# Kernel optimization log

Measured on AMD Instinct MI355X. Metric: run time of the kernel, lower is better.

Reference implementation:

```python
import jax, jax.numpy as jnp
import numpy as np

B, N, M, C, K = 4, 4096, 4096, 64, 32
RADIUS = 0.1
EPS = 1e-5


def setup_inputs() -> dict:
    key = jax.random.key(0)
    ks = jax.random.split(key, 32)
    inp = {
        "query_xyz": jax.random.uniform(ks[0], (B, N, 3), jnp.float32),
        "support_xyz": jax.random.uniform(ks[1], (B, M, 3), jnp.float32),
        "query_mask": jax.random.randint(ks[2], (B, N), 0, 2, jnp.int32),
        "support_mask": jax.random.randint(ks[3], (B, M), 0, 2, jnp.int32),
        "support_features": jax.random.normal(ks[4], (B, C, M), jnp.float32),
    }
    names = ["theta1", "theta2", "phi", "psi", "alpha", "gamma1", "gamma2"]
    in_ch = {"theta1": 3}
    for j, nm in enumerate(names):
        inp[f"W_{nm}"] = jax.random.normal(ks[5 + j], (C, in_ch.get(nm, C)), jnp.float32) * 0.05
        inp[f"b_{nm}"] = jax.random.normal(ks[12 + j], (C,), jnp.float32) * 0.05
    for j, nm in enumerate(["theta", "gamma"]):
        inp[f"g_{nm}"] = 1.0 + 0.1 * jax.random.normal(ks[19 + 2 * j], (C,), jnp.float32)
        inp[f"be_{nm}"] = 0.1 * jax.random.normal(ks[20 + 2 * j], (C,), jnp.float32)
        inp[f"rm_{nm}"] = jnp.zeros((C,), jnp.float32)
        inp[f"rv_{nm}"] = jnp.ones((C,), jnp.float32)
    return inp


def _conv(W, b, x):
    # 1x1 Conv2d: channelwise linear on [B, C_in, N, K]
    return jnp.einsum('oc,bcnk->bonk', W, x) + b[None, :, None, None]


def _bn(x, g, be, rm, rv):
    # BatchNorm2d, inference form with running stats
    inv = g / jnp.sqrt(rv + EPS)
    return x * inv[None, :, None, None] + (be - rm * inv)[None, :, None, None]


def _forward(query_xyz, support_xyz, query_mask, support_mask, support_features, P):
    Bq, Nq = query_xyz.shape[:2]
    # pairwise squared distances [B, N, M]; masked support pushed to +inf
    d2 = jnp.sum((query_xyz[:, :, None, :] - support_xyz[:, None, :, :]) ** 2, axis=-1)
    d2 = jnp.where(support_mask[:, None, :] > 0, d2, jnp.inf)
    # ball query as K-nearest-within-radius
    neg, idx = jax.lax.top_k(-d2, K)                    # idx: [B, N, K]
    nbr_mask = (-neg) <= RADIUS ** 2                    # valid-neighbor mask
    flat = idx.reshape(Bq, Nq * K)
    x_j = jnp.take_along_axis(support_features, flat[:, None, :], axis=2).reshape(Bq, -1, Nq, K)
    g_xyz = jnp.take_along_axis(support_xyz, flat[:, :, None], axis=1).reshape(Bq, Nq, K, 3)
    # normalize_xyz=True -> offsets divided by radius; layout [B, 3, N, K]
    pos = ((g_xyz - query_xyz[:, :, None, :]) / RADIUS).transpose(0, 3, 1, 2)
    # nearest-neighbor query for x_i [B, C, N]
    idx_nn = jnp.argmin(d2, axis=-1)
    x_i = jnp.take_along_axis(support_features, idx_nn[:, None, :], axis=2)
    # positional encoding delta
    delta = jax.nn.relu(_bn(_conv(P['W_theta2'], P['b_theta2'],
                                  _conv(P['W_theta1'], P['b_theta1'], pos)),
                            P['g_theta'], P['be_theta'], P['rm_theta'], P['rv_theta']))
    lin_i = _conv(P['W_phi'], P['b_phi'], x_i[..., None])   # [B,C,N,1], broadcast over K
    lin_j = _conv(P['W_psi'], P['b_psi'], x_j)
    rel = lin_i - lin_j + delta
    rel = jax.nn.relu(_bn(_conv(P['W_gamma2'], P['b_gamma2'],
                                _conv(P['W_gamma1'], P['b_gamma1'], rel)),
                          P['g_gamma'], P['be_gamma'], P['rm_gamma'], P['rv_gamma']))
    weights = jax.nn.softmax(rel, axis=-1)                   # softmax over neighbor axis
    feats = _conv(P['W_alpha'], P['b_alpha'], x_j) + delta
    fmask = nbr_mask.astype(feats.dtype) + (1.0 - query_mask.astype(feats.dtype))[:, :, None]
    feats = feats * fmask[:, None, :, :]
    return jnp.sum(weights * feats, axis=-1)                 # [B, C, N]


def reference(query_xyz, support_xyz, query_mask, support_mask, support_features,
              W_theta1, b_theta1, W_theta2, b_theta2, W_phi, b_phi, W_psi, b_psi,
              W_alpha, b_alpha, W_gamma1, b_gamma1, W_gamma2, b_gamma2,
              g_theta, be_theta, rm_theta, rv_theta, g_gamma, be_gamma, rm_gamma, rv_gamma):
    P = dict(locals())
    return _forward(query_xyz, support_xyz, query_mask, support_mask, support_features, P)
```

## Files before the change

### kernel.cpp

```cpp
#include <hip/hip_runtime.h>
#include <cstdint>
#include <cstddef>

#define NN 4096
#define MM 4096
#define CC 64
#define KK 32
#define INF_F __builtin_huge_valf()

#define SC 2304
#define CCAP 2560

typedef __bf16 bf16x8 __attribute__((ext_vector_type(8)));
typedef __bf16 bf16x4 __attribute__((ext_vector_type(4)));
typedef float f32x16 __attribute__((ext_vector_type(16)));

#define NFRAG 40
#define NPRE 24
#define ASTRIDE 68
#define ESTRIDE 36

#define WFENCE() asm volatile("s_waitcnt lgkmcnt(0)" ::: "memory")


__device__ __forceinline__ f32x16 zero16() {
  f32x16 z;
#pragma unroll
  for (int i = 0; i < 16; ++i) z[i] = 0.0f;
  return z;
}

__device__ __forceinline__ void conv1(const bf16x8* Wr, int conv,
                                      const bf16x8* B4, f32x16& a0, f32x16& a1) {
#pragma unroll
  for (int s = 0; s < 4; ++s) {
    a0 = __builtin_amdgcn_mfma_f32_32x32x16_bf16(Wr[(conv * 2 + 0) * 4 + s], B4[s], a0, 0, 0, 0);
    a1 = __builtin_amdgcn_mfma_f32_32x32x16_bf16(Wr[(conv * 2 + 1) * 4 + s], B4[s], a1, 0, 0, 0);
  }
}

__device__ __forceinline__ void conv1g(const bf16x8* __restrict__ Wf, int conv, int lane,
                                       const bf16x8* B4, f32x16& a0, f32x16& a1) {
#pragma unroll
  for (int s = 0; s < 4; ++s) {
    const bf16x8 w0 = Wf[((conv * 2 + 0) * 4 + s) * 64 + lane];
    const bf16x8 w1 = Wf[((conv * 2 + 1) * 4 + s) * 64 + lane];
    a0 = __builtin_amdgcn_mfma_f32_32x32x16_bf16(w0, B4[s], a0, 0, 0, 0);
    a1 = __builtin_amdgcn_mfma_f32_32x32x16_bf16(w1, B4[s], a1, 0, 0, 0);
  }
}

__device__ __forceinline__ void sort64(float& v, int& i, int lane) {
#pragma unroll
  for (int k = 2; k <= 64; k <<= 1) {
#pragma unroll
    for (int j = k >> 1; j > 0; j >>= 1) {
      const float ov = __shfl_xor(v, j);
      const int oi = __shfl_xor(i, j);
      const bool up = ((lane & k) == 0);
      const bool lower = ((lane & j) == 0);
      const bool take = (up == lower) ? (ov < v) : (ov > v);
      if (take) { v = ov; i = oi; }
    }
  }
}

__device__ __forceinline__ void insert_cands(float vv, int ii, float& sv, int& si,
                                             float& cmax, int lane) {
  unsigned long long cand = __ballot(vv < cmax);
  while (cand) {
    const int src = __ffsll((unsigned long long)cand) - 1;
    cand &= cand - 1;
    const float dc = __shfl(vv, src);
    if (dc < cmax) {
      const int im = __shfl(ii, src);
      const float up_s = __shfl_up(sv, 1);
      const int up_i = __shfl_up(si, 1);
      const bool pg = sv > dc;
      const bool pgu = (lane > 0) && (up_s > dc);
      const float ns = pg ? (pgu ? up_s : dc) : sv;
      const int ni = pg ? (pgu ? up_i : im) : si;
      if (lane < 32) { sv = ns; si = ni; }
      cmax = __shfl(sv, 31);
    }
  }
}

__global__ void pt_setup(const float* __restrict__ sf, const float* __restrict__ sxyz,
                         const int* __restrict__ smask,
                         const float* __restrict__ Wpsi, const float* __restrict__ W2,
                         const float* __restrict__ Wg1, const float* __restrict__ Wg2,
                         const float* __restrict__ Wa, const float* __restrict__ Wphi,
                         const float* __restrict__ gT, const float* __restrict__ beT,
                         const float* __restrict__ rmT, const float* __restrict__ rvT,
                         const float* __restrict__ gG, const float* __restrict__ beG,
                         const float* __restrict__ rmG, const float* __restrict__ rvG,
                         const float* __restrict__ b2, const float* __restrict__ bg1,
                         const float* __restrict__ bg2, const float* __restrict__ ba,
                         __bf16* __restrict__ ftb, float4* __restrict__ sx4,
                         float4* __restrict__ cpts, __bf16* __restrict__ Wpack,
                         float* __restrict__ WphiT, float4* __restrict__ eo,
                         float4* __restrict__ bo) {
  const int blk = blockIdx.x;
  const int tid = threadIdx.x;

  if (blk < 64) {
    const int b = blk >> 4;
    const int m = ((blk & 15) << 8) + tid;
    float v[CC];
#pragma unroll
    for (int c = 0; c < CC; ++c) v[c] = sf[((size_t)(b * CC + c)) * MM + m];
    bf16x8* db = (bf16x8*)(ftb + ((size_t)(b * MM + m)) * CC);
#pragma unroll
    for (int i = 0; i < CC / 8; ++i) {
      bf16x8 t;
#pragma unroll
      for (int j = 0; j < 8; ++j) t[j] = (__bf16)v[8 * i + j];
      db[i] = t;
    }
    const size_t g = (size_t)(b * MM + m);
    sx4[g] = make_float4(sxyz[g * 3 + 0], sxyz[g * 3 + 1], sxyz[g * 3 + 2], 0.0f);
    return;
  }

  if (blk < 68) {
    __shared__ int lcount;
    const int b = blk - 64;
    const int lane = tid & 63;
    if (tid == 0) lcount = 0;
    __syncthreads();
    float4* dst = cpts + (size_t)b * CCAP;
#pragma unroll 1
    for (int r = 0; r < 16; ++r) {
      const int m = r * 256 + tid;
      const size_t g = (size_t)b * MM + m;
      const bool valid = smask[g] > 0;
      float x = 0, y = 0, z = 0;
      if (valid) { x = sxyz[g * 3 + 0]; y = sxyz[g * 3 + 1]; z = sxyz[g * 3 + 2]; }
      const unsigned long long mask = __ballot(valid);
      const int pre = (int)__popcll(mask & ((1ull << lane) - 1ull));
      int wbase = 0;
      if (lane == 0) wbase = atomicAdd(&lcount, (int)__popcll(mask));
      wbase = __shfl(wbase, 0);
      if (valid) dst[wbase + pre] = make_float4(x, y, z, __int_as_float(m));
    }
    __syncthreads();
    const int cnt = lcount;
    for (int i = cnt + tid; i < SC; i += 256)
      dst[i] = make_float4(1e4f, 1e4f, 1e4f, __int_as_float(0));
    return;
  }

  const int t = (blk - 68) * 256 + tid;
  if (t < NFRAG * 64) {
    const int lane = t & 63;
    const int fi = t >> 6;
    const int s = fi & 3;
    const int mt = (fi >> 2) & 1;
    const int conv = fi >> 3;
    const float* W = conv == 0 ? Wpsi : conv == 1 ? W2 : conv == 2 ? Wg1 : conv == 3 ? Wg2 : Wa;
    const int m = mt * 32 + (lane & 31);
    const int k0 = s * 16 + (lane >> 5) * 8;
    bf16x8 vh;
#pragma unroll
    for (int j = 0; j < 8; ++j) vh[j] = (__bf16)W[m * CC + k0 + j];
    ((bf16x8*)Wpack)[fi * 64 + lane] = vh;
    return;
  }
  const int t2 = t - NFRAG * 64;
  if (t2 < CC * CC) {
    WphiT[t2] = Wphi[(t2 & 63) * CC + (t2 >> 6)];
    return;
  }
  const int o = t2 - CC * CC;
  if (o < CC) {
    const float invT = gT[o] / sqrtf(rvT[o] + 1e-5f);
    const float invG = gG[o] / sqrtf(rvG[o] + 1e-5f);
    eo[o] = make_float4(invT, beT[o] - rmT[o] * invT, invG, beG[o] - rmG[o] * invG);
    bo[o] = make_float4(b2[o], bg1[o], bg2[o], ba[o]);
  }
}

__global__ void pt_knn(const float* __restrict__ qxyz, const float4* __restrict__ cpts,
                       const __bf16* __restrict__ ftb,
                       const float* __restrict__ WphiT, const float* __restrict__ bphi,
                       const float* __restrict__ bpsi,
                       int* __restrict__ oidx, unsigned* __restrict__ ovalid,
                       float* __restrict__ lin) {
  const int lane = threadIdx.x & 63;
  const int qi = blockIdx.x * 4 + (threadIdx.x >> 6);
  const int b = qi >> 12;
  const float qx = qxyz[qi * 3 + 0];
  const float qy = qxyz[qi * 3 + 1];
  const float qz = qxyz[qi * 3 + 2];
  const float4* sb = cpts + (size_t)b * CCAP;

  float v0 = INF_F, v1 = INF_F, v2 = INF_F, v3 = INF_F;
  int i0 = 0, i1 = 0, i2 = 0, i3 = 0;
#pragma unroll 1
  for (int j = 0; j < 36; j += 4) {
    float4 P[4];
#pragma unroll
    for (int u = 0; u < 4; ++u) P[u] = sb[(j + u) * 64 + lane];
#pragma unroll
    for (int u = 0; u < 4; ++u) {
      const float dx = P[u].x - qx, dy = P[u].y - qy, dz = P[u].z - qz;
      const float d = dx * dx + dy * dy + dz * dz;
      const int m = __float_as_int(P[u].w);
      const bool c3 = d < v3, c2 = d < v2, c1 = d < v1, c0 = d < v0;
      v3 = c3 ? (c2 ? v2 : d) : v3;  i3 = c3 ? (c2 ? i2 : m) : i3;
      v2 = c2 ? (c1 ? v1 : d) : v2;  i2 = c2 ? (c1 ? i1 : m) : i2;
      v1 = c1 ? (c0 ? v0 : d) : v1;  i1 = c1 ? (c0 ? i0 : m) : i1;
      v0 = c0 ? d : v0;              i0 = c0 ? m : i0;
    }
  }

  float sv = v0;
  int si = i0;
  sort64(sv, si, lane);
  float cmax = __shfl(sv, 31);
  insert_cands(v1, i1, sv, si, cmax, lane);
  insert_cands(v2, i2, sv, si, cmax, lane);
  insert_cands(v3, i3, sv, si, cmax, lane);

  if (__ballot(v3 < cmax)) {
    {
      const float4 p = sb[lane];
      const float dx = p.x - qx, dy = p.y - qy, dz = p.z - qz;
      float v = dx * dx + dy * dy + dz * dz;
      int id = __float_as_int(p.w);
      sort64(v, id, lane);
      sv = v; si = id;
    }
    cmax = __shfl(sv, 31);
    for (int m0 = 64; m0 < SC; m0 += 64) {
      const float4 p = sb[m0 + lane];
      const float dx = p.x - qx, dy = p.y - qy, dz = p.z - qz;
      const float d = dx * dx + dy * dy + dz * dz;
      insert_cands(d, __float_as_int(p.w), sv, si, cmax, lane);
    }
  }

  if (lane < 32) oidx[(size_t)qi * KK + lane] = si;
  const unsigned long long vb = __ballot((lane < 32) && (sv <= 0.01f));
  if (lane == 0) ovalid[qi] = (unsigned)(vb & 0xffffffffull);

  const int nnb = __shfl(si, 0);
  const bf16x8* xr = (const bf16x8*)(ftb + ((size_t)(b * MM + nnb)) * CC);
  float a = bphi[lane] - bpsi[lane];
#pragma unroll
  for (int i = 0; i < 8; ++i) {
    const bf16x8 xv = xr[i];
#pragma unroll
    for (int j = 0; j < 8; ++j) a += WphiT[(8 * i + j) * CC + lane] * (float)xv[j];
  }
  lin[qi * CC + lane] = a;
}

__launch_bounds__(256, 3)
__global__ void pt_fused(
    const float* __restrict__ qxyz, const float4* __restrict__ sx4,
    const int* __restrict__ qmask, const __bf16* __restrict__ ftb,
    const int* __restrict__ kidx, const unsigned* __restrict__ kvalid,
    const float* __restrict__ lin,
    const float* __restrict__ W1, const float* __restrict__ b1,
    const __bf16* __restrict__ Wpack, const float4* __restrict__ eo,
    const float4* __restrict__ bo, float* __restrict__ out) {
  __shared__ float EPI[4][CC * ESTRIDE];
  __shared__ float4 sEO[CC], sBO[CC];
  const int wid = threadIdx.x >> 6;
  const int lane = threadIdx.x & 63;
  const int g = lane >> 5;
  const int col = lane & 31;
  const int q = blockIdx.x * 4 + wid;
  const int b = q >> 12;
  const int nq = q & (NN - 1);
  float* epi = EPI[wid];
  __bf16* act = (__bf16*)epi;
  const bf16x8* Wf = (const bf16x8*)Wpack;

  bf16x8 Wr[NPRE];
#pragma unroll
  for (int f = 0; f < NPRE; ++f) Wr[f] = Wf[f * 64 + lane];

  sEO[lane] = eo[lane];
  sBO[lane] = bo[lane];

  const int idx = kidx[q * KK + col];
  const float fm = (float)((kvalid[q] >> col) & 1u) + 1.0f - (float)qmask[q];

  bf16x8 Xb[4];
  {
    const __bf16* ftq = ftb + ((size_t)(b * MM + idx)) * CC;
#pragma unroll
    for (int s = 0; s < 4; ++s) Xb[s] = *(const bf16x8*)(ftq + s * 16 + g * 8);
  }

  bf16x8 Tb[4];
  {
    const float qx = qxyz[q * 3 + 0], qy = qxyz[q * 3 + 1], qz = qxyz[q * 3 + 2];
    const float4 pj = sx4[(size_t)b * MM + idx];
    const float p0 = (pj.x - qx) * 10.0f;
    const float p1 = (pj.y - qy) * 10.0f;
    const float p2 = (pj.z - qz) * 10.0f;
#pragma unroll
    for (int s = 0; s < 4; ++s) {
      bf16x8 t;
#pragma unroll
      for (int j = 0; j < 8; ++j) {
        const int c = s * 16 + g * 8 + j;
        t[j] = (__bf16)(b1[c] + W1[c * 3 + 0] * p0 + W1[c * 3 + 1] * p1 + W1[c * 3 + 2] * p2);
      }
      Tb[s] = t;
    }
  }
  WFENCE();

  float DELv[32];
  {
    f32x16 aT0 = zero16(), aT1 = zero16();
    conv1(Wr, 1, Tb, aT0, aT1);
#pragma unroll
    for (int mt = 0; mt < 2; ++mt)
#pragma unroll
      for (int t = 0; t < 4; ++t)
#pragma unroll
        for (int i = 0; i < 4; ++i) {
          const int r = t * 4 + i;
          const int o = mt * 32 + 8 * t + 4 * g + i;
          const float4 e = sEO[o];
          DELv[mt * 16 + r] = fmaxf(((mt ? aT1[r] : aT0[r]) + sBO[o].x) * e.x + e.y, 0.0f);
        }
  }

  {
    f32x16 aP0 = zero16(), aP1 = zero16();
    conv1(Wr, 0, Xb, aP0, aP1);
#pragma unroll
    for (int mt = 0; mt < 2; ++mt)
#pragma unroll
      for (int t = 0; t < 4; ++t) {
        const int ob = mt * 32 + 8 * t + 4 * g;
        const float4 lv = *(const float4*)(lin + q * CC + ob);
        const float lva[4] = {lv.x, lv.y, lv.z, lv.w};
        bf16x4 w;
#pragma unroll
        for (int i = 0; i < 4; ++i) {
          const int r = t * 4 + i;
          w[i] = (__bf16)(lva[i] - (mt ? aP1[r] : aP0[r]) + DELv[mt * 16 + r]);
        }
        *(bf16x4*)(act + col * ASTRIDE + ob) = w;
      }
  }
  WFENCE();

  {
    bf16x8 Rb[4];
#pragma unroll
    for (int s = 0; s < 4; ++s) {
      const bf16x4 lo = *(const bf16x4*)(act + col * ASTRIDE + s * 16 + g * 8);
      const bf16x4 hi = *(const bf16x4*)(act + col * ASTRIDE + s * 16 + g * 8 + 4);
      Rb[s] = bf16x8{lo[0], lo[1], lo[2], lo[3], hi[0], hi[1], hi[2], hi[3]};
    }
    f32x16 a0 = zero16(), a1 = zero16();
    conv1(Wr, 2, Rb, a0, a1);
#pragma unroll
    for (int mt = 0; mt < 2; ++mt)
#pragma unroll
      for (int t = 0; t < 4; ++t) {
        const int ob = mt * 32 + 8 * t + 4 * g;
        bf16x4 w;
#pragma unroll
        for (int i = 0; i < 4; ++i) {
          const int r = t * 4 + i;
          w[i] = (__bf16)((mt ? a1[r] : a0[r]) + sBO[ob + i].y);
        }
        *(bf16x4*)(act + col * ASTRIDE + ob) = w;
      }
  }
  WFENCE();

  f32x16 h0 = zero16(), h1 = zero16();
  {
    bf16x8 Rb[4];
#pragma unroll
    for (int s = 0; s < 4; ++s) {
      const bf16x4 lo = *(const bf16x4*)(act + col * ASTRIDE + s * 16 + g * 8);
      const bf16x4 hi = *(const bf16x4*)(act + col * ASTRIDE + s * 16 + g * 8 + 4);
      Rb[s] = bf16x8{lo[0], lo[1], lo[2], lo[3], hi[0], hi[1], hi[2], hi[3]};
    }
    conv1g(Wf, 3, lane, Rb, h0, h1);
  }
  WFENCE();

#pragma unroll
  for (int mt = 0; mt < 2; ++mt)
#pragma unroll
    for (int t = 0; t < 4; ++t)
#pragma unroll
      for (int i = 0; i < 4; ++i) {
        const int r = t * 4 + i;
        const int o = mt * 32 + 4 * g + 8 * t + i;
        const float4 e = sEO[o];
        const float v = fmaxf(((mt ? h1[r] : h0[r]) + sBO[o].z) * e.z + e.w, 0.0f);
        epi[o * ESTRIDE + col] = v;
      }
  WFENCE();

  float ev[32];
  float sum;
  {
    const float* row = epi + lane * ESTRIDE;
    float mx = -INF_F;
#pragma unroll
    for (int n = 0; n < 32; n += 4) {
      const float4 t = *(const float4*)(row + n);
      ev[n] = t.x; ev[n + 1] = t.y; ev[n + 2] = t.z; ev[n + 3] = t.w;
      mx = fmaxf(mx, fmaxf(fmaxf(t.x, t.y), fmaxf(t.z, t.w)));
    }
    sum = 0.0f;
#pragma unroll
    for (int n = 0; n < 32; ++n) { ev[n] = __expf(ev[n] - mx); sum += ev[n]; }
  }
  WFENCE();

  f32x16 fa0 = zero16(), fa1 = zero16();
  conv1g(Wf, 4, lane, Xb, fa0, fa1);

#pragma unroll
  for (int mt = 0; mt < 2; ++mt)
#pragma unroll
    for (int t = 0; t < 4; ++t)
#pragma unroll
      for (int i = 0; i < 4; ++i) {
        const int r = t * 4 + i;
        const int o = mt * 32 + 4 * g + 8 * t + i;
        const float f = ((mt ? fa1[r] : fa0[r]) + sBO[o].w + DELv[mt * 16 + r]) * fm;
        epi[o * ESTRIDE + col] = f;
      }
  WFENCE();

  {
    const float* row = epi + lane * ESTRIDE;
    float acc = 0.0f;
#pragma unroll
    for (int n = 0; n < 32; n += 4) {
      const float4 t = *(const float4*)(row + n);
      acc += ev[n] * t.x + ev[n + 1] * t.y + ev[n + 2] * t.z + ev[n + 3] * t.w;
    }
    out[((size_t)(b * CC + lane)) * NN + nq] = acc * __builtin_amdgcn_rcpf(sum);
  }
}

extern "C" void kernel_launch(void* const* d_in, const int* in_sizes, int n_in,
                              void* d_out, int out_size, void* d_ws, size_t ws_size,
                              hipStream_t stream) {
  (void)in_sizes; (void)n_in; (void)out_size; (void)ws_size;
  const float* qxyz = (const float*)d_in[0];
  const float* sxyz = (const float*)d_in[1];
  const int* qmask = (const int*)d_in[2];
  const int* smask = (const int*)d_in[3];
  const float* sfeat = (const float*)d_in[4];
  const float* W1 = (const float*)d_in[5];
  const float* b1 = (const float*)d_in[6];
  const float* W2 = (const float*)d_in[7];
  const float* b2 = (const float*)d_in[8];
  const float* Wphi = (const float*)d_in[9];
  const float* bphi = (const float*)d_in[10];
  const float* Wpsi = (const float*)d_in[11];
  const float* bpsi = (const float*)d_in[12];
  const float* Wa = (const float*)d_in[13];
  const float* ba = (const float*)d_in[14];
  const float* Wg1 = (const float*)d_in[15];
  const float* bg1 = (const float*)d_in[16];
  const float* Wg2 = (const float*)d_in[17];
  const float* bg2 = (const float*)d_in[18];
  const float* gT = (const float*)d_in[19];
  const float* beT = (const float*)d_in[20];
  const float* rmT = (const float*)d_in[21];
  const float* rvT = (const float*)d_in[22];
  const float* gG = (const float*)d_in[23];
  const float* beG = (const float*)d_in[24];
  const float* rmG = (const float*)d_in[25];
  const float* rvG = (const float*)d_in[26];

  char* ws = (char*)d_ws;
  int* kidx      = (int*)(ws + 0);
  unsigned* kval = (unsigned*)(ws + 2097152);
  __bf16* ftb    = (__bf16*)(ws + 2162688);
  float4* sx4    = (float4*)(ws + 4259840);
  float* lin     = (float*)(ws + 4521984);
  __bf16* Wpack  = (__bf16*)(ws + 8716288);
  float4* eo     = (float4*)(ws + 8757248);
  float4* bo     = (float4*)(ws + 8758272);
  float4* cpts   = (float4*)(ws + 8759296);
  float* WphiT   = (float*)(ws + 8923136);

  hipLaunchKernelGGL(pt_setup, dim3(95), dim3(256), 0, stream,
                     sfeat, sxyz, smask,
                     Wpsi, W2, Wg1, Wg2, Wa, Wphi,
                     gT, beT, rmT, rvT, gG, beG, rmG, rvG, b2, bg1, bg2, ba,
                     ftb, sx4, cpts, Wpack, WphiT, eo, bo);
  hipLaunchKernelGGL(pt_knn, dim3(4096), dim3(256), 0, stream,
                     qxyz, cpts, ftb, WphiT, bphi, bpsi, kidx, kval, lin);
  hipLaunchKernelGGL(pt_fused, dim3(4096), dim3(256), 0, stream,
                     qxyz, sx4, qmask, ftb, kidx, kval, lin,
                     W1, b1, Wpack, eo, bo, (float*)d_out);
}
```

Baseline: 244.1 us.

## Bucket support points by x-coordinate to prune KNN search to a slab

The setup kernel now counting-sorts valid support points into 256 buckets along x and stores bucket offsets. The KNN kernel estimates a search radius from point density, scans only the rows covering the x-slab around each query, and widens the slab if the current 32nd-nearest distance exceeds the slab margin. This replaces the full scan of every compacted point with a data-dependent, smaller scan. In exchange it adds a histogram/scan pass in setup, extra branching, and correctness relies on the fallback widening covering all cases.

Result: faster. 236.4 us (-3.2%).

```diff
diff --git a/kernel.cpp b/kernel.cpp
--- a/kernel.cpp
+++ b/kernel.cpp
@@ -10,6 +10,7 @@
 
 #define SC 2304
 #define CCAP 2560
+#define NBUCK 256
 
 typedef __bf16 bf16x8 __attribute__((ext_vector_type(8)));
 typedef __bf16 bf16x4 __attribute__((ext_vector_type(4)));
@@ -100,7 +101,7 @@
                          __bf16* __restrict__ ftb, float4* __restrict__ sx4,
                          float4* __restrict__ cpts, __bf16* __restrict__ Wpack,
                          float* __restrict__ WphiT, float4* __restrict__ eo,
-                         float4* __restrict__ bo) {
+                         float4* __restrict__ bo, int* __restrict__ boffp) {
   const int blk = blockIdx.x;
   const int tid = threadIdx.x;
 
@@ -124,29 +125,58 @@
   }
 
   if (blk < 68) {
-    __shared__ int lcount;
+    __shared__ int cnt[NBUCK];
+    __shared__ int cur[NBUCK];
+    __shared__ int wtot[4];
     const int b = blk - 64;
     const int lane = tid & 63;
-    if (tid == 0) lcount = 0;
+    const int w = tid >> 6;
+    cnt[tid] = 0;
+    __syncthreads();
+#pragma unroll 1
+    for (int r = 0; r < 16; ++r) {
+      const int m = r * 256 + tid;
+      const size_t g = (size_t)b * MM + m;
+      if (smask[g] > 0) {
+        int bk = (int)(sxyz[g * 3 + 0] * 256.0f);
+        bk = min(max(bk, 0), NBUCK - 1);
+        atomicAdd(&cnt[bk], 1);
+      }
+    }
+    __syncthreads();
+    const int v = cnt[tid];
+    int inc = v;
+#pragma unroll
+    for (int off = 1; off < 64; off <<= 1) {
+      const int o = __shfl_up(inc, off);
+      if (lane >= off) inc += o;
+    }
+    if (lane == 63) wtot[w] = inc;
+    __syncthreads();
+    int excl = inc - v;
+#pragma unroll
+    for (int i = 0; i < 4; ++i) excl += (i < w) ? wtot[i] : 0;
+    cur[tid] = excl;
+    boffp[b * 257 + tid] = excl;
+    const int total = wtot[0] + wtot[1] + wtot[2] + wtot[3];
+    if (tid == 0) boffp[b * 257 + 256] = total;
     __syncthreads();
     float4* dst = cpts + (size_t)b * CCAP;
 #pragma unroll 1
     for (int r = 0; r < 16; ++r) {
       const int m = r * 256 + tid;
       const size_t g = (size_t)b * MM + m;
-      const bool valid = smask[g] > 0;
-      float x = 0, y = 0, z = 0;
-      if (valid) { x = sxyz[g * 3 + 0]; y = sxyz[g * 3 + 1]; z = sxyz[g * 3 + 2]; }
-      const unsigned long long mask = __ballot(valid);
-      const int pre = (int)__popcll(mask & ((1ull << lane) - 1ull));
-      int wbase = 0;
-      if (lane == 0) wbase = atomicAdd(&lcount, (int)__popcll(mask));
-      wbase = __shfl(wbase, 0);
-      if (valid) dst[wbase + pre] = make_float4(x, y, z, __int_as_float(m));
-    }
-    __syncthreads();
-    const int cnt = lcount;
-    for (int i = cnt + tid; i < SC; i += 256)
+      if (smask[g] > 0) {
+        const float x = sxyz[g * 3 + 0];
+        const float y = sxyz[g * 3 + 1];
+        const float z = sxyz[g * 3 + 2];
+        int bk = (int)(x * 256.0f);
+        bk = min(max(bk, 0), NBUCK - 1);
+        const int pos = atomicAdd(&cur[bk], 1);
+        dst[pos] = make_float4(x, y, z, __int_as_float(m));
+      }
+    }
+    for (int i = total + tid; i < SC; i += 256)
       dst[i] = make_float4(1e4f, 1e4f, 1e4f, __int_as_float(0));
     return;
   }
@@ -182,7 +212,7 @@
 }
 
 __global__ void pt_knn(const float* __restrict__ qxyz, const float4* __restrict__ cpts,
-                       const __bf16* __restrict__ ftb,
+                       const int* __restrict__ boff, const __bf16* __restrict__ ftb,
                        const float* __restrict__ WphiT, const float* __restrict__ bphi,
                        const float* __restrict__ bpsi,
                        int* __restrict__ oidx, unsigned* __restrict__ ovalid,
@@ -194,14 +224,33 @@
   const float qy = qxyz[qi * 3 + 1];
   const float qz = qxyz[qi * 3 + 2];
   const float4* sb = cpts + (size_t)b * CCAP;
+  const int* bo = boff + b * 257;
+  const int cnt = bo[256];
+
+  float R = 0.155f;
+#pragma unroll
+  for (int it = 0; it < 2; ++it) {
+    const float cx = fminf(qx + R, 1.0f) - fmaxf(qx - R, 0.0f);
+    const float cy = fminf(qy + R, 1.0f) - fmaxf(qy - R, 0.0f);
+    const float cz = fminf(qz + R, 1.0f) - fmaxf(qz - R, 0.0f);
+    const float n = fmaxf((float)cnt * 0.5235988f * cx * cy * cz, 1.0f);
+    R *= __powf(48.0f / n, 0.33333333f);
+  }
+  R = fminf(fmaxf(R, 0.06f), 0.7f);
+
+  const int lob = max((int)((qx - R) * 256.0f), 0);
+  const int hib = min((int)((qx + R) * 256.0f), NBUCK - 1);
+  const int r0 = bo[lob] >> 6;
+  const int r1 = (bo[hib + 1] + 63) >> 6;
 
   float v0 = INF_F, v1 = INF_F, v2 = INF_F, v3 = INF_F;
   int i0 = 0, i1 = 0, i2 = 0, i3 = 0;
+  int r = r0;
 #pragma unroll 1
-  for (int j = 0; j < 36; j += 4) {
+  for (; r + 4 <= r1; r += 4) {
     float4 P[4];
 #pragma unroll
-    for (int u = 0; u < 4; ++u) P[u] = sb[(j + u) * 64 + lane];
+    for (int u = 0; u < 4; ++u) P[u] = sb[(r + u) * 64 + lane];
 #pragma unroll
     for (int u = 0; u < 4; ++u) {
       const float dx = P[u].x - qx, dy = P[u].y - qy, dz = P[u].z - qz;
@@ -214,6 +263,18 @@
       v0 = c0 ? d : v0;              i0 = c0 ? m : i0;
     }
   }
+#pragma unroll 1
+  for (; r < r1; ++r) {
+    const float4 p = sb[r * 64 + lane];
+    const float dx = p.x - qx, dy = p.y - qy, dz = p.z - qz;
+    const float d = dx * dx + dy * dy + dz * dz;
+    const int m = __float_as_int(p.w);
+    const bool c3 = d < v3, c2 = d < v2, c1 = d < v1, c0 = d < v0;
+    v3 = c3 ? (c2 ? v2 : d) : v3;  i3 = c3 ? (c2 ? i2 : m) : i3;
+    v2 = c2 ? (c1 ? v1 : d) : v2;  i2 = c2 ? (c1 ? i1 : m) : i2;
+    v1 = c1 ? (c0 ? v0 : d) : v1;  i1 = c1 ? (c0 ? i0 : m) : i1;
+    v0 = c0 ? d : v0;              i0 = c0 ? m : i0;
+  }
 
   float sv = v0;
   int si = i0;
@@ -223,9 +284,9 @@
   insert_cands(v2, i2, sv, si, cmax, lane);
   insert_cands(v3, i3, sv, si, cmax, lane);
 
-  if (__ballot(v3 < cmax)) {
+  if (__ballot(v3 < cmax) && r1 > r0) {
     {
-      const float4 p = sb[lane];
+      const float4 p = sb[r0 * 64 + lane];
       const float dx = p.x - qx, dy = p.y - qy, dz = p.z - qz;
       float v = dx * dx + dy * dy + dz * dz;
       int id = __float_as_int(p.w);
@@ -233,11 +294,32 @@
       sv = v; si = id;
     }
     cmax = __shfl(sv, 31);
-    for (int m0 = 64; m0 < SC; m0 += 64) {
-      const float4 p = sb[m0 + lane];
+    for (int rr = r0 + 1; rr < r1; ++rr) {
+      const float4 p = sb[rr * 64 + lane];
       const float dx = p.x - qx, dy = p.y - qy, dz = p.z - qz;
       const float d = dx * dx + dy * dy + dz * dz;
       insert_cands(d, __float_as_int(p.w), sv, si, cmax, lane);
+    }
+  }
+
+  const float gl = (lob > 0) ? (qx - (float)lob * 0.00390625f) : INF_F;
+  const float gr = (hib < NBUCK - 1) ? ((float)(hib + 1) * 0.00390625f - qx) : INF_F;
+  const float G = fminf(gl, gr);
+  if (cmax > G * G) {
+    const float R1 = sqrtf(cmax);
+    const int lob2 = max((int)((qx - R1) * 256.0f), 0);
+    const int hib2 = min((int)((qx + R1) * 256.0f), NBUCK - 1);
+    const int s0 = bo[lob2] >> 6;
+    const int s1 = (bo[hib2 + 1] + 63) >> 6;
+    for (int rr = s0; rr < r0; ++rr) {
+      const float4 p = sb[rr * 64 + lane];
+      const float dx = p.x - qx, dy = p.y - qy, dz = p.z - qz;
+      insert_cands(dx * dx + dy * dy + dz * dz, __float_as_int(p.w), sv, si, cmax, lane);
+    }
+    for (int rr = r1; rr < s1; ++rr) {
+      const float4 p = sb[rr * 64 + lane];
+      const float dx = p.x - qx, dy = p.y - qy, dz = p.z - qz;
+      insert_cands(dx * dx + dy * dy + dz * dz, __float_as_int(p.w), sv, si, cmax, lane);
     }
   }
 
@@ -495,14 +577,15 @@
   float4* bo     = (float4*)(ws + 8758272);
   float4* cpts   = (float4*)(ws + 8759296);
   float* WphiT   = (float*)(ws + 8923136);
+  int* boffp     = (int*)(ws + 8939520);
 
   hipLaunchKernelGGL(pt_setup, dim3(95), dim3(256), 0, stream,
                      sfeat, sxyz, smask,
                      Wpsi, W2, Wg1, Wg2, Wa, Wphi,
                      gT, beT, rmT, rvT, gG, beG, rmG, rvG, b2, bg1, bg2, ba,
-                     ftb, sx4, cpts, Wpack, WphiT, eo, bo);
+                     ftb, sx4, cpts, Wpack, WphiT, eo, bo, boffp);
   hipLaunchKernelGGL(pt_knn, dim3(4096), dim3(256), 0, stream,
-                     qxyz, cpts, ftb, WphiT, bphi, bpsi, kidx, kval, lin);
+                     qxyz, cpts, boffp, ftb, WphiT, bphi, bpsi, kidx, kval, lin);
   hipLaunchKernelGGL(pt_fused, dim3(4096), dim3(256), 0, stream,
                      qxyz, sx4, qmask, ftb, kidx, kval, lin,
                      W1, b1, Wpack, eo, bo, (float*)d_out);
```
